# Performance work log

Measured on AMD Instinct MI355X. Metric: run time of the kernel, lower is better.

## Reference

```python
import jax, jax.numpy as jnp
import numpy as np

DT = 0.01
SIM_STEPS = 10_000_000
G = jnp.array([0.0, -9.81], dtype=jnp.float32)  # gravity, matches Ball.g


def setup_inputs() -> dict:
    key = jax.random.key(0)
    k_pos, k_vel = jax.random.split(key)
    return {
        "ball_mass": jnp.ones((), dtype=jnp.float32),  # unused by the math, kept for signature fidelity
        "ball_initial_position": jax.random.normal(k_pos, (2,), dtype=jnp.float32),
        "ball_initial_velocity": jax.random.normal(k_vel, (2,), dtype=jnp.float32),  # nn.Parameter
    }


def reference(ball_mass, ball_initial_position, ball_initial_velocity):
    # Faithful semi-implicit-Euler-style recurrence:
    #   pos <- pos + vel*dt ; vel <- vel + g*dt ; record pos
    # trajectory[0] is the initial position, trajectory[1:] are the updated positions.
    def step(carry, _):
        pos, vel = carry
        pos = pos + vel * DT
        vel = vel + G * DT
        return (pos, vel), pos

    _, traj = jax.lax.scan(
        step, (ball_initial_position, ball_initial_velocity), None, length=SIM_STEPS - 1
    )  # traj: [SIM_STEPS-1, 2]
    return jnp.concatenate([ball_initial_position[None, :], traj], axis=0)  # [SIM_STEPS, 2]
```

## Files before the change

### kernel.cpp

```cpp
#include <hip/hip_runtime.h>
#include <stdint.h>


static constexpr long long NSTEPS = 10000000LL;
static constexpr long long NPOLY  = 4000000LL;
static constexpr long long NS     = 8000000LL;
static constexpr long long KDIR   = 64;
static constexpr int SEGCAP = 384;
static constexpr int RUNCAP = 96;

typedef float f4_native __attribute__((ext_vector_type(4)));

__device__ __forceinline__ bool same_binade_f32(float a, float b) {
    return (((__float_as_uint(a) ^ __float_as_uint(b)) & 0xFF800000u) == 0u);
}
__device__ __forceinline__ unsigned expfield(float v) {
    return (__float_as_uint(v) >> 23) & 0xFFu;
}
__device__ __forceinline__ float pow2f(int e) {
    return __uint_as_float((unsigned)(e + 127) << 23);
}
__device__ __forceinline__ double pow2d(int e) {
    return __longlong_as_double(((long long)(e + 1023)) << 52);
}
__device__ __forceinline__ void nt_store(float4* p, float4 v) {
    f4_native nv;
    nv.x = v.x; nv.y = v.y; nv.z = v.z; nv.w = v.w;
    __builtin_nontemporal_store(nv, (f4_native*)p);
}

__global__ __launch_bounds__(256, 4) void fused(
        const float* __restrict__ pos0, const float* __restrict__ vel0,
        float4* __restrict__ out, long long npairs)
{
    __shared__ int    s_m[SEGCAP + 1];
    __shared__ double s_V[SEGCAP], s_c[SEGCAP], s_P[SEGCAP], s_dP[SEGCAP];
    __shared__ float  s_Vf[SEGCAP], s_cdt[SEGCAP], s_Pf[SEGCAP];
    __shared__ int    r_n[RUNCAP];
    __shared__ double r_p[RUNCAP], r_i[RUNCAP];
    __shared__ float  r_pf[RUNCAP], r_if[RUNCAP];
    __shared__ int    s_nseg, s_bad, s_nrun;
    __shared__ long long s_mstop;
    __shared__ double s_v64, s_p64;

    const int tid  = threadIdx.x;
    const int lane = tid & 63;
    const int wv   = tid >> 6;

    const long long per = (npairs + (long long)gridDim.x - 1) / (long long)gridDim.x;
    const long long i0 = (long long)blockIdx.x * per;
    long long i1 = i0 + per; if (i1 > npairs) i1 = npairs;
    if (i0 >= npairs) return;
    const long long row0 = 2 * i0;
    const long long row1 = 2 * i1;
    const long long mstop = row1 < NSTEPS ? row1 : NSTEPS;

    const float dtf  = 0.01f;
    const float gdtf = __fmul_rn(-9.81f, dtf);
    const double dtd = (double)dtf, gcd = (double)gdtf, gdtd = gcd;
    const double p0y = (double)pos0[1], v0y = (double)vel0[1];

    int k_tie;
    {
        unsigned gbits = __float_as_uint(gdtf);
        unsigned mant = (gbits & 0x7FFFFFu) | 0x800000u;
        int tz = __ffs((int)mant) - 1;
        int E = (int)((gbits >> 23) & 0xFFu) - 127 - 23 + tz;
        k_tie = E + 25;
    }

    if (tid == 0) { s_nseg = 0; s_nrun = 0; s_mstop = 0; s_bad = 0; }
    __syncthreads();

    if (wv == 0 && row1 > NPOLY) {
        double V = v0y, P = p0y;
        for (int t = 0; t < (int)KDIR; ++t) {
            const float vf = (float)V;
            P += dtd * V;
            V = (double)__fadd_rn(vf, gdtf);
        }
        if (lane == 0) { s_v64 = V; s_p64 = P; }

        bool bad = false;
        long long m = KDIR;
        int nseg = 0;
        while (m < mstop && nseg < SEGCAP - 2) {
            const float vf = (float)V;
            const unsigned ef = expfield(vf);
            bad = bad | ((double)vf != V) | !(vf < 0.0f) | (ef == 0u) | (ef == 0xFFu);
            if (bad) break;
            const int k = (int)ef - 126;
            const float vn1 = __fadd_rn(vf, gdtf);
            const double c = (double)vn1 - V;
            if (!(c < 0.0)) { bad = true; break; }
            const long long rem = mstop - m;

            long long T = 1;
            if (k != k_tie) {
                const double inv_ulp = pow2d(24 - k);
                const double g  = -V * inv_ulp;
                const double q  = -gcd * inv_ulp;
                const double cg = -c * inv_ulp;
                const double lim = 16777216.0;
                float t0f = __fdividef((float)(lim - g - q), (float)cg);
                const long long Th = (long long)t0f;
                const long long Tc = Th - 31 + (long long)lane;
                const bool valid = (Tc >= 1) && (Tc <= rem)
                                && (g + (double)(Tc - 1) * cg + q < lim);
                const unsigned long long msk = __ballot(valid);
                if (msk) T = Th - 31 + (long long)(63 - __clzll(msk));
                else     T = (Th - 31 > rem) ? rem : 1;
                if (T < 1) T = 1;
                if (T > rem) T = rem;
            }
            if (lane == 0) { s_m[nseg] = (int)m; s_V[nseg] = V; s_c[nseg] = c; }
            ++nseg;
            V += (double)T * c;
            m += T;
        }
        bad = bad | (m < mstop);
        if (lane == 0) {
            s_bad = bad ? 1 : 0;
            s_nseg = nseg;
            s_mstop = m;
            s_m[nseg] = 0x7fffffff;
        }
    }
    __syncthreads();

    if (wv == 0 && s_bad && row1 > NPOLY) {
        double V = s_v64, P = s_p64;
        long long m = KDIR;
        int nseg = 0;
        while (m < mstop && nseg < SEGCAP) {
            const float vf  = (float)V;
            const float vn1 = __fadd_rn(vf, gdtf);
            const double c  = (double)vn1 - V;
            const long long rem = mstop - m;
            long long Lb = rem;
            const float cf = (float)c;
            const unsigned ef = expfield(vf);
            if (vf == 0.0f || ef == 0u) {
                Lb = 64;
            } else if (cf != 0.0f) {
                const int k = (int)ef - 126;
                float s = vf < 0.0f ? -1.0f : 1.0f;
                float B = ((vf < 0.0f) == (cf < 0.0f)) ? s * pow2f(k) : s * pow2f(k - 1);
                float r = __fdividef(B - vf, cf);
                if (r >= 0.0f && r < 4.0e9f) Lb = (long long)r + 1;
            }
            long long Lhi = Lb + 2;
            if (Lhi > rem) Lhi = rem;
            if (Lhi < 1) Lhi = 1;

            long long L = 1;
            {
                const long long candL = Lhi - 63 + (long long)lane;
                bool valid = false;
                if (candL >= 1) {
                    const double ve = V + (double)(candL - 1) * c;
                    const float vef = (float)ve;
                    const float vn2 = __fadd_rn(vef, gdtf);
                    valid = ((double)vef == ve)
                         && same_binade_f32(vef, vf)
                         && ((double)vn2 - ve == c);
                }
                const unsigned long long msk = __ballot(valid);
                if (msk) L = Lhi - 63 + (long long)(63 - __clzll(msk));
            }
            if (L < 1) L = 1;
            if (L > rem) L = rem;

            if (lane == 0) { s_m[nseg] = (int)m; s_V[nseg] = V; s_c[nseg] = c; s_P[nseg] = P; }
            ++nseg;
            P += dtd * ((double)L * V + c * ((double)L * (double)(L - 1) * 0.5));
            V += (double)L * c;
            m += L;
        }
        if (lane == 0) { s_nseg = nseg; s_mstop = m; s_m[nseg] = 0x7fffffff; }
    }
    __syncthreads();

    if (!s_bad && row1 > NPOLY && s_nseg > 0) {
        const int nseg = s_nseg;
        for (int j = tid; j < nseg; j += 256) {
            const long long mj = s_m[j];
            const long long me = (j + 1 < nseg) ? (long long)s_m[j + 1] : s_mstop;
            const double len = (double)(me - mj);
            s_dP[j] = dtd * (len * s_V[j] + s_c[j] * (len * (len - 1.0) * 0.5));
        }
        __syncthreads();
        if (tid == 0) {
            double P = s_p64;
            for (int j = 0; j < nseg; ++j) { s_P[j] = P; P += s_dP[j]; }
        }
    }
    __syncthreads();

    if (wv == 0 && row1 > NS && s_mstop >= NS && s_nseg > 0) {
        const int nseg = s_nseg;
        const long long mbuilt = s_mstop;
        int lo = 0, hi = nseg - 1;
        while (lo < hi) { int mid = (lo + hi + 1) >> 1;
                          if ((long long)s_m[mid] <= NS) lo = mid; else hi = mid - 1; }
        int jj = lo;
        const double t0 = (double)(NS - s_m[jj]);
        double vel = s_V[jj] + t0 * s_c[jj];
        double P2  = s_P[jj] + dtd * (t0 * s_V[jj] + s_c[jj] * (t0 * (t0 - 1.0) * 0.5));
        double pos = (double)(float)P2;
        long long n = NS;
        int nrun = 0;
        long long nend = (row1 < NSTEPS - 1) ? row1 : (NSTEPS - 1);
        if (nend > mbuilt) nend = mbuilt;
        while (n < nend && nrun < RUNCAP) {
            while (s_m[jj + 1] <= (int)n) ++jj;
            const double cv = s_c[jj];
            long long Lcap = (long long)s_m[jj + 1] - n;
            if (Lcap > mbuilt - n) Lcap = mbuilt - n;
            const long long rem = (NSTEPS - 1) - n;
            if (Lcap > rem) Lcap = rem;

            const float pf = (float)pos;
            const float vf2 = (float)vel;
            const float dstep = __fmul_rn(vf2, dtf);
            const float pn1 = __fadd_rn(pf, dstep);
            const double inc = (double)pn1 - pos;

            long long La = Lcap, Lc = Lcap;
            const float incf = (float)inc;
            const unsigned efp = expfield(pf);
            if (pf == 0.0f || efp == 0u) {
                La = 64;
            } else if (incf != 0.0f) {
                const int k = (int)efp - 126;
                float s = pf < 0.0f ? -1.0f : 1.0f;
                float B = ((pf < 0.0f) == (incf < 0.0f)) ? s * pow2f(k) : s * pow2f(k - 1);
                float r = __fdividef(B - pf, incf);
                if (r >= 0.0f && r < 4.0e9f) { La = (long long)r - 1; if (La < 0) La = 0; }
            }
            const double dd = cv * dtd;
            if (dd != 0.0 && pf != 0.0f && efp != 0u) {
                const int k = (int)efp - 126;
                if (k - 24 > -126) {
                    const float ulpf = pow2f(k - 24);
                    const double d0 = (double)dstep;
                    const double T = inc + (dd < 0.0 ? -0.5 : 0.5) * (double)ulpf;
                    float r = __fdividef((float)(T - d0), (float)dd);
                    if (r >= 0.0f && r < 4.0e9f) { Lc = (long long)r + 2; if (Lc < 1) Lc = 1; }
                }
            }
            long long Lhi = La < Lc ? La : Lc;
            Lhi += 3;
            if (Lhi > Lcap) Lhi = Lcap;
            if (Lhi < 1) Lhi = 1;

            long long L = 1;
            {
                const long long candL = Lhi - 63 + (long long)lane;
                bool valid = false;
                if (candL >= 1) {
                    const double pe = pos + (double)(candL - 1) * inc;
                    const double ve = vel + (double)(candL - 1) * cv;
                    const float pef = (float)pe;
                    const float vef = (float)ve;
                    const float d2  = __fmul_rn(vef, dtf);
                    const float pn2 = __fadd_rn(pef, d2);
                    valid = ((double)pef == pe)
                         && same_binade_f32(pef, pf)
                         && ((double)vef == ve)
                         && ((double)pn2 - pe == inc);
                }
                const unsigned long long msk = __ballot(valid);
                if (msk) L = Lhi - 63 + (long long)(63 - __clzll(msk));
            }
            if (L < 1) L = 1;
            if (L > Lcap) L = Lcap;
            if (L < 1) L = 1;

            if (lane == 0) { r_n[nrun] = (int)n; r_p[nrun] = pos; r_i[nrun] = inc; }
            ++nrun;
            pos += (double)L * inc;
            vel += (double)L * cv;
            n += L;
        }
        if (lane == 0) s_nrun = nrun;
    }
    __syncthreads();

    {
        const int nseg = s_nseg, nrun = s_nrun;
        for (int i = tid; i < nseg; i += 256) {
            s_Vf[i]  = (float)s_V[i];
            s_cdt[i] = (float)(dtd * s_c[i]);
            s_Pf[i]  = (float)s_P[i];
        }
        for (int i = tid; i < nrun; i += 256) {
            r_pf[i] = (float)r_p[i];
            r_if[i] = (float)r_i[i];
        }
    }
    __syncthreads();

    const int nseg = s_nseg;
    const int nrun = s_nrun;
    const float pxf = pos0[0];
    const float cxf = __fmul_rn(vel0[0], dtf);
    const float pyf = (float)p0y;
    const float vyf = (float)v0y;
    const float q2f = (float)(dtd * gdtd);

    const long long ii = i0 + tid;
    if (ii >= i1) return;

    int mode = 3, jf = 0, rf = 0;
    if (row1 <= NPOLY) {
        mode = 0;
    } else if (row0 >= NS && nrun > 0) {
        int rlo = 0, rhi = nrun - 1;
        const int t0 = (int)row0;
        while (rlo < rhi) { int mid = (rlo + rhi + 1) >> 1; if (r_n[mid] <= t0) rlo = mid; else rhi = mid - 1; }
        rf = rlo;
        if (rf + 1 >= nrun || (long long)r_n[rf + 1] >= row1) mode = 2;
    } else if (row0 >= NPOLY && row1 <= NS && nseg > 0) {
        int lo = 0, hi = nseg - 1;
        const int t0 = (int)row0;
        while (lo < hi) { int mid = (lo + hi + 1) >> 1; if (s_m[mid] <= t0) lo = mid; else hi = mid - 1; }
        jf = lo;
        if ((long long)s_m[jf + 1] >= row1) mode = 1;
    }

    if (mode == 0) {
        const float C = 0.5f * q2f;
        const float B = dtf * vyf - C;
        const float A = pyf;
        for (long long i = ii; i < i1; i += blockDim.x) {
            const float mf0 = (float)(2 * i), mf1 = mf0 + 1.0f;
            float4 o;
            o.x = fmaf(mf0, cxf, pxf);
            o.z = fmaf(mf1, cxf, pxf);
            o.y = fmaf(mf0, fmaf(mf0, C, B), A);
            o.w = fmaf(mf1, fmaf(mf1, C, B), A);
            nt_store(&out[i], o);
        }
    } else if (mode == 1) {
        const float C = 0.5f * s_cdt[jf];
        const float B = dtf * s_Vf[jf] - C;
        const float A = s_Pf[jf];
        const int mj = s_m[jf];
        for (long long i = ii; i < i1; i += blockDim.x) {
            const float t0 = (float)(int)(2 * i - mj), t1 = t0 + 1.0f;
            const float mf0 = (float)(2 * i), mf1 = mf0 + 1.0f;
            float4 o;
            o.x = fmaf(mf0, cxf, pxf);
            o.z = fmaf(mf1, cxf, pxf);
            o.y = fmaf(t0, fmaf(t0, C, B), A);
            o.w = fmaf(t1, fmaf(t1, C, B), A);
            nt_store(&out[i], o);
        }
    } else if (mode == 2) {
        const float A = r_pf[rf], Bv = r_if[rf];
        const int rn0 = r_n[rf];
        for (long long i = ii; i < i1; i += blockDim.x) {
            const float t0 = (float)(int)(2 * i - rn0), t1 = t0 + 1.0f;
            const float mf0 = (float)(2 * i), mf1 = mf0 + 1.0f;
            float4 o;
            o.x = fmaf(mf0, cxf, pxf);
            o.z = fmaf(mf1, cxf, pxf);
            o.y = fmaf(t0, Bv, A);
            o.w = fmaf(t1, Bv, A);
            nt_store(&out[i], o);
        }
    } else {
        int j = 0, r = 0;
        if (nseg > 0) {
            const int t0 = (int)(2 * ii);
            int lo = 0, hi = nseg - 1;
            while (lo < hi) { int mid = (lo + hi + 1) >> 1; if (s_m[mid] <= t0) lo = mid; else hi = mid - 1; }
            j = lo;
            if (nrun > 0) {
                int rlo = 0, rhi = nrun - 1;
                while (rlo < rhi) { int mid = (rlo + rhi + 1) >> 1; if (r_n[mid] <= t0) rlo = mid; else rhi = mid - 1; }
                r = rlo;
            }
        }
        for (long long i = ii; i < i1; i += blockDim.x) {
            const long long m0 = 2 * i, m1 = m0 + 1;
            const float mf0 = (float)m0, mf1 = (float)m1;
            float4 o;
            o.x = fmaf(mf0, cxf, pxf);
            o.z = fmaf(mf1, cxf, pxf);
            const int t0 = (int)m0;
            if (m1 < NPOLY) {
                const float C = 0.5f * q2f;
                const float B = dtf * vyf - C;
                o.y = fmaf(mf0, fmaf(mf0, C, B), pyf);
                o.w = fmaf(mf1, fmaf(mf1, C, B), pyf);
            } else if (m1 < NS || nrun <= 0) {
                while (s_m[j + 1] <= t0) ++j;
                float t = (float)(int)(m0 - s_m[j]);
                o.y = s_Pf[j] + dtf * (t * s_Vf[j]) + s_cdt[j] * (t * (t - 1.0f) * 0.5f);
                const int j1 = (s_m[j + 1] <= (int)m1) ? j + 1 : j;
                t = (float)(int)(m1 - s_m[j1]);
                o.w = s_Pf[j1] + dtf * (t * s_Vf[j1]) + s_cdt[j1] * (t * (t - 1.0f) * 0.5f);
            } else {
                while (r + 1 < nrun && r_n[r + 1] <= t0) ++r;
                o.y = r_pf[r] + (float)(int)(m0 - r_n[r]) * r_if[r];
                const int r1 = (r + 1 < nrun && r_n[r + 1] <= (int)m1) ? r + 1 : r;
                o.w = r_pf[r1] + (float)(int)(m1 - r_n[r1]) * r_if[r1];
            }
            nt_store(&out[i], o);
        }
    }
}

extern "C" void kernel_launch(void* const* d_in, const int* in_sizes, int n_in,
                              void* d_out, int out_size, void* d_ws, size_t ws_size,
                              hipStream_t stream) {
    const float* pos0 = (const float*)d_in[1];
    const float* vel0 = (const float*)d_in[2];

    const long long npairs = (long long)out_size / 4;
    fused<<<1024, 256, 0, stream>>>(pos0, vel0, (float4*)d_out, npairs);
}
```

Measured before the change: 35.13 us.

## Give each block a poly slice and a late slice, overlapping poly stores with segment build

Each block now owns one slice of the closed-form polynomial region and one slice of the later segment-based region, instead of a single contiguous range. Wave 0 builds the segment and run tables while the other three waves write the block's polynomial slice, so table construction overlaps with global stores. The fallback path and the prefix sum of P are merged into wave 0's single pass, which removes several __syncthreads and the s_dP scratch array. The cost is that every block now runs the serial segment-building loop, and the prefix sum is done by a single lane.

```diff
diff --git a/kernel.cpp b/kernel.cpp
--- a/kernel.cpp
+++ b/kernel.cpp
@@ -8,6 +8,8 @@
 static constexpr long long KDIR   = 64;
 static constexpr int SEGCAP = 384;
 static constexpr int RUNCAP = 96;
+static constexpr long long PF4 = NPOLY / 2;
+static constexpr long long LF4 = (NSTEPS - NPOLY) / 2;
 
 typedef float f4_native __attribute__((ext_vector_type(4)));
 
@@ -34,26 +36,24 @@
         float4* __restrict__ out, long long npairs)
 {
     __shared__ int    s_m[SEGCAP + 1];
-    __shared__ double s_V[SEGCAP], s_c[SEGCAP], s_P[SEGCAP], s_dP[SEGCAP];
+    __shared__ double s_V[SEGCAP], s_c[SEGCAP], s_P[SEGCAP];
     __shared__ float  s_Vf[SEGCAP], s_cdt[SEGCAP], s_Pf[SEGCAP];
     __shared__ int    r_n[RUNCAP];
     __shared__ double r_p[RUNCAP], r_i[RUNCAP];
     __shared__ float  r_pf[RUNCAP], r_if[RUNCAP];
-    __shared__ int    s_nseg, s_bad, s_nrun;
+    __shared__ int    s_nseg, s_nrun;
     __shared__ long long s_mstop;
-    __shared__ double s_v64, s_p64;
 
     const int tid  = threadIdx.x;
     const int lane = tid & 63;
     const int wv   = tid >> 6;
-
-    const long long per = (npairs + (long long)gridDim.x - 1) / (long long)gridDim.x;
-    const long long i0 = (long long)blockIdx.x * per;
-    long long i1 = i0 + per; if (i1 > npairs) i1 = npairs;
-    if (i0 >= npairs) return;
-    const long long row0 = 2 * i0;
-    const long long row1 = 2 * i1;
-    const long long mstop = row1 < NSTEPS ? row1 : NSTEPS;
+    const long long G = gridDim.x;
+    const long long b = blockIdx.x;
+
+    const long long pb0 = (b * PF4) / G,       pb1 = ((b + 1) * PF4) / G;
+    const long long lb0 = PF4 + (b * LF4) / G, lb1 = PF4 + ((b + 1) * LF4) / G;
+    const long long lrow0 = 2 * lb0, lrow1 = 2 * lb1;
+    const long long mstop = lrow1 < NSTEPS ? lrow1 : NSTEPS;
 
     const float dtf  = 0.01f;
     const float gdtf = __fmul_rn(-9.81f, dtf);
@@ -69,17 +69,22 @@
         k_tie = E + 25;
     }
 
-    if (tid == 0) { s_nseg = 0; s_nrun = 0; s_mstop = 0; s_bad = 0; }
-    __syncthreads();
-
-    if (wv == 0 && row1 > NPOLY) {
+    const float pxf = pos0[0];
+    const float cxf = __fmul_rn(vel0[0], dtf);
+    const float pyf = (float)p0y;
+    const float vyf = (float)v0y;
+    const float q2f = (float)(dtd * gdtd);
+    const float Cq  = 0.5f * q2f;
+    const float Bq  = dtf * vyf - Cq;
+
+    if (wv == 0) {
         double V = v0y, P = p0y;
         for (int t = 0; t < (int)KDIR; ++t) {
             const float vf = (float)V;
             P += dtd * V;
             V = (double)__fadd_rn(vf, gdtf);
         }
-        if (lane == 0) { s_v64 = V; s_p64 = P; }
+        const double v64 = V, p64 = P;
 
         bool bad = false;
         long long m = KDIR;
@@ -119,171 +124,171 @@
             m += T;
         }
         bad = bad | (m < mstop);
+        long long built = m;
+
+        if (bad) {
+            V = v64; P = p64;
+            m = KDIR;
+            nseg = 0;
+            while (m < mstop && nseg < SEGCAP) {
+                const float vf  = (float)V;
+                const float vn1 = __fadd_rn(vf, gdtf);
+                const double c  = (double)vn1 - V;
+                const long long rem = mstop - m;
+                long long Lb = rem;
+                const float cf = (float)c;
+                const unsigned ef = expfield(vf);
+                if (vf == 0.0f || ef == 0u) {
+                    Lb = 64;
+                } else if (cf != 0.0f) {
+                    const int k = (int)ef - 126;
+                    float s = vf < 0.0f ? -1.0f : 1.0f;
+                    float B = ((vf < 0.0f) == (cf < 0.0f)) ? s * pow2f(k) : s * pow2f(k - 1);
+                    float r = __fdividef(B - vf, cf);
+                    if (r >= 0.0f && r < 4.0e9f) Lb = (long long)r + 1;
+                }
+                long long Lhi = Lb + 2;
+                if (Lhi > rem) Lhi = rem;
+                if (Lhi < 1) Lhi = 1;
+
+                long long L = 1;
+                {
+                    const long long candL = Lhi - 63 + (long long)lane;
+                    bool valid = false;
+                    if (candL >= 1) {
+                        const double ve = V + (double)(candL - 1) * c;
+                        const float vef = (float)ve;
+                        const float vn2 = __fadd_rn(vef, gdtf);
+                        valid = ((double)vef == ve)
+                             && same_binade_f32(vef, vf)
+                             && ((double)vn2 - ve == c);
+                    }
+                    const unsigned long long msk = __ballot(valid);
+                    if (msk) L = Lhi - 63 + (long long)(63 - __clzll(msk));
+                }
+                if (L < 1) L = 1;
+                if (L > rem) L = rem;
+
+                if (lane == 0) { s_m[nseg] = (int)m; s_V[nseg] = V; s_c[nseg] = c; s_P[nseg] = P; }
+                ++nseg;
+                P += dtd * ((double)L * V + c * ((double)L * (double)(L - 1) * 0.5));
+                V += (double)L * c;
+                m += L;
+            }
+            built = m;
+        } else if (lane == 0 && nseg > 0) {
+            double Pp = p64;
+            for (int j = 0; j < nseg; ++j) {
+                s_P[j] = Pp;
+                const long long mj = s_m[j];
+                const long long me = (j + 1 < nseg) ? (long long)s_m[j + 1] : built;
+                const double len = (double)(me - mj);
+                Pp += dtd * (len * s_V[j] + s_c[j] * (len * (len - 1.0) * 0.5));
+            }
+        }
         if (lane == 0) {
-            s_bad = bad ? 1 : 0;
             s_nseg = nseg;
-            s_mstop = m;
+            s_mstop = built;
             s_m[nseg] = 0x7fffffff;
-        }
-    }
-    __syncthreads();
-
-    if (wv == 0 && s_bad && row1 > NPOLY) {
-        double V = s_v64, P = s_p64;
-        long long m = KDIR;
-        int nseg = 0;
-        while (m < mstop && nseg < SEGCAP) {
-            const float vf  = (float)V;
-            const float vn1 = __fadd_rn(vf, gdtf);
-            const double c  = (double)vn1 - V;
-            const long long rem = mstop - m;
-            long long Lb = rem;
-            const float cf = (float)c;
-            const unsigned ef = expfield(vf);
-            if (vf == 0.0f || ef == 0u) {
-                Lb = 64;
-            } else if (cf != 0.0f) {
-                const int k = (int)ef - 126;
-                float s = vf < 0.0f ? -1.0f : 1.0f;
-                float B = ((vf < 0.0f) == (cf < 0.0f)) ? s * pow2f(k) : s * pow2f(k - 1);
-                float r = __fdividef(B - vf, cf);
-                if (r >= 0.0f && r < 4.0e9f) Lb = (long long)r + 1;
-            }
-            long long Lhi = Lb + 2;
-            if (Lhi > rem) Lhi = rem;
-            if (Lhi < 1) Lhi = 1;
-
-            long long L = 1;
-            {
-                const long long candL = Lhi - 63 + (long long)lane;
-                bool valid = false;
-                if (candL >= 1) {
-                    const double ve = V + (double)(candL - 1) * c;
-                    const float vef = (float)ve;
-                    const float vn2 = __fadd_rn(vef, gdtf);
-                    valid = ((double)vef == ve)
-                         && same_binade_f32(vef, vf)
-                         && ((double)vn2 - ve == c);
+            s_nrun = 0;
+        }
+
+        if (lrow1 > NS && built >= NS && nseg > 0) {
+            int lo = 0, hi = nseg - 1;
+            while (lo < hi) { int mid = (lo + hi + 1) >> 1;
+                              if ((long long)s_m[mid] <= NS) lo = mid; else hi = mid - 1; }
+            int jj = lo;
+            const double t0 = (double)(NS - s_m[jj]);
+            double vel = s_V[jj] + t0 * s_c[jj];
+            double P2  = s_P[jj] + dtd * (t0 * s_V[jj] + s_c[jj] * (t0 * (t0 - 1.0) * 0.5));
+            double pos = (double)(float)P2;
+            long long n = NS;
+            int nrun = 0;
+            long long nend = (lrow1 < NSTEPS - 1) ? lrow1 : (NSTEPS - 1);
+            if (nend > built) nend = built;
+            while (n < nend && nrun < RUNCAP) {
+                while (s_m[jj + 1] <= (int)n) ++jj;
+                const double cv = s_c[jj];
+                long long Lcap = (long long)s_m[jj + 1] - n;
+                if (Lcap > built - n) Lcap = built - n;
+                const long long rem = (NSTEPS - 1) - n;
+                if (Lcap > rem) Lcap = rem;
+
+                const float pf = (float)pos;
+                const float vf2 = (float)vel;
+                const float dstep = __fmul_rn(vf2, dtf);
+                const float pn1 = __fadd_rn(pf, dstep);
+                const double inc = (double)pn1 - pos;
+
+                long long La = Lcap, Lc = Lcap;
+                const float incf = (float)inc;
+                const unsigned efp = expfield(pf);
+                if (pf == 0.0f || efp == 0u) {
+                    La = 64;
+                } else if (incf != 0.0f) {
+                    const int k = (int)efp - 126;
+                    float s = pf < 0.0f ? -1.0f : 1.0f;
+                    float B = ((pf < 0.0f) == (incf < 0.0f)) ? s * pow2f(k) : s * pow2f(k - 1);
+                    float r = __fdividef(B - pf, incf);
+                    if (r >= 0.0f && r < 4.0e9f) { La = (long long)r - 1; if (La < 0) La = 0; }
                 }
-                const unsigned long long msk = __ballot(valid);
-                if (msk) L = Lhi - 63 + (long long)(63 - __clzll(msk));
-            }
-            if (L < 1) L = 1;
-            if (L > rem) L = rem;
-
-            if (lane == 0) { s_m[nseg] = (int)m; s_V[nseg] = V; s_c[nseg] = c; s_P[nseg] = P; }
-            ++nseg;
-            P += dtd * ((double)L * V + c * ((double)L * (double)(L - 1) * 0.5));
-            V += (double)L * c;
-            m += L;
-        }
-        if (lane == 0) { s_nseg = nseg; s_mstop = m; s_m[nseg] = 0x7fffffff; }
-    }
-    __syncthreads();
-
-    if (!s_bad && row1 > NPOLY && s_nseg > 0) {
-        const int nseg = s_nseg;
-        for (int j = tid; j < nseg; j += 256) {
-            const long long mj = s_m[j];
-            const long long me = (j + 1 < nseg) ? (long long)s_m[j + 1] : s_mstop;
-            const double len = (double)(me - mj);
-            s_dP[j] = dtd * (len * s_V[j] + s_c[j] * (len * (len - 1.0) * 0.5));
-        }
-        __syncthreads();
-        if (tid == 0) {
-            double P = s_p64;
-            for (int j = 0; j < nseg; ++j) { s_P[j] = P; P += s_dP[j]; }
-        }
-    }
-    __syncthreads();
-
-    if (wv == 0 && row1 > NS && s_mstop >= NS && s_nseg > 0) {
-        const int nseg = s_nseg;
-        const long long mbuilt = s_mstop;
-        int lo = 0, hi = nseg - 1;
-        while (lo < hi) { int mid = (lo + hi + 1) >> 1;
-                          if ((long long)s_m[mid] <= NS) lo = mid; else hi = mid - 1; }
-        int jj = lo;
-        const double t0 = (double)(NS - s_m[jj]);
-        double vel = s_V[jj] + t0 * s_c[jj];
-        double P2  = s_P[jj] + dtd * (t0 * s_V[jj] + s_c[jj] * (t0 * (t0 - 1.0) * 0.5));
-        double pos = (double)(float)P2;
-        long long n = NS;
-        int nrun = 0;
-        long long nend = (row1 < NSTEPS - 1) ? row1 : (NSTEPS - 1);
-        if (nend > mbuilt) nend = mbuilt;
-        while (n < nend && nrun < RUNCAP) {
-            while (s_m[jj + 1] <= (int)n) ++jj;
-            const double cv = s_c[jj];
-            long long Lcap = (long long)s_m[jj + 1] - n;
-            if (Lcap > mbuilt - n) Lcap = mbuilt - n;
-            const long long rem = (NSTEPS - 1) - n;
-            if (Lcap > rem) Lcap = rem;
-
-            const float pf = (float)pos;
-            const float vf2 = (float)vel;
-            const float dstep = __fmul_rn(vf2, dtf);
-            const float pn1 = __fadd_rn(pf, dstep);
-            const double inc = (double)pn1 - pos;
-
-            long long La = Lcap, Lc = Lcap;
-            const float incf = (float)inc;
-            const unsigned efp = expfield(pf);
-            if (pf == 0.0f || efp == 0u) {
-                La = 64;
-            } else if (incf != 0.0f) {
-                const int k = (int)efp - 126;
-                float s = pf < 0.0f ? -1.0f : 1.0f;
-                float B = ((pf < 0.0f) == (incf < 0.0f)) ? s * pow2f(k) : s * pow2f(k - 1);
-                float r = __fdividef(B - pf, incf);
-                if (r >= 0.0f && r < 4.0e9f) { La = (long long)r - 1; if (La < 0) La = 0; }
-            }
-            const double dd = cv * dtd;
-            if (dd != 0.0 && pf != 0.0f && efp != 0u) {
-                const int k = (int)efp - 126;
-                if (k - 24 > -126) {
-                    const float ulpf = pow2f(k - 24);
-                    const double d0 = (double)dstep;
-                    const double T = inc + (dd < 0.0 ? -0.5 : 0.5) * (double)ulpf;
-                    float r = __fdividef((float)(T - d0), (float)dd);
-                    if (r >= 0.0f && r < 4.0e9f) { Lc = (long long)r + 2; if (Lc < 1) Lc = 1; }
+                const double dd = cv * dtd;
+                if (dd != 0.0 && pf != 0.0f && efp != 0u) {
+                    const int k = (int)efp - 126;
+                    if (k - 24 > -126) {
+                        const float ulpf = pow2f(k - 24);
+                        const double d0 = (double)dstep;
+                        const double T = inc + (dd < 0.0 ? -0.5 : 0.5) * (double)ulpf;
+                        float r = __fdividef((float)(T - d0), (float)dd);
+                        if (r >= 0.0f && r < 4.0e9f) { Lc = (long long)r + 2; if (Lc < 1) Lc = 1; }
+                    }
                 }
-            }
-            long long Lhi = La < Lc ? La : Lc;
-            Lhi += 3;
-            if (Lhi > Lcap) Lhi = Lcap;
-            if (Lhi < 1) Lhi = 1;
-
-            long long L = 1;
-            {
-                const long long candL = Lhi - 63 + (long long)lane;
-                bool valid = false;
-                if (candL >= 1) {
-                    const double pe = pos + (double)(candL - 1) * inc;
-                    const double ve = vel + (double)(candL - 1) * cv;
-                    const float pef = (float)pe;
-                    const float vef = (float)ve;
-                    const float d2  = __fmul_rn(vef, dtf);
-                    const float pn2 = __fadd_rn(pef, d2);
-                    valid = ((double)pef == pe)
-                         && same_binade_f32(pef, pf)
-                         && ((double)vef == ve)
-                         && ((double)pn2 - pe == inc);
+                long long Lhi = La < Lc ? La : Lc;
+                Lhi += 3;
+                if (Lhi > Lcap) Lhi = Lcap;
+                if (Lhi < 1) Lhi = 1;
+
+                long long L = 1;
+                {
+                    const long long candL = Lhi - 63 + (long long)lane;
+                    bool valid = false;
+                    if (candL >= 1) {
+                        const double pe = pos + (double)(candL - 1) * inc;
+                        const double ve = vel + (double)(candL - 1) * cv;
+                        const float pef = (float)pe;
+                        const float vef = (float)ve;
+                        const float d2  = __fmul_rn(vef, dtf);
+                        const float pn2 = __fadd_rn(pef, d2);
+                        valid = ((double)pef == pe)
+                             && same_binade_f32(pef, pf)
+                             && ((double)vef == ve)
+                             && ((double)pn2 - pe == inc);
+                    }
+                    const unsigned long long msk = __ballot(valid);
+                    if (msk) L = Lhi - 63 + (long long)(63 - __clzll(msk));
                 }
-                const unsigned long long msk = __ballot(valid);
-                if (msk) L = Lhi - 63 + (long long)(63 - __clzll(msk));
-            }
-            if (L < 1) L = 1;
-            if (L > Lcap) L = Lcap;
-            if (L < 1) L = 1;
-
-            if (lane == 0) { r_n[nrun] = (int)n; r_p[nrun] = pos; r_i[nrun] = inc; }
-            ++nrun;
-            pos += (double)L * inc;
-            vel += (double)L * cv;
-            n += L;
-        }
-        if (lane == 0) s_nrun = nrun;
+                if (L < 1) L = 1;
+                if (L > Lcap) L = Lcap;
+                if (L < 1) L = 1;
+
+                if (lane == 0) { r_n[nrun] = (int)n; r_p[nrun] = pos; r_i[nrun] = inc; }
+                ++nrun;
+                pos += (double)L * inc;
+                vel += (double)L * cv;
+                n += L;
+            }
+            if (lane == 0) s_nrun = nrun;
+        }
+    } else {
+        for (long long i = pb0 + (tid - 64); i < pb1; i += 192) {
+            const float mf0 = (float)(2 * i), mf1 = mf0 + 1.0f;
+            float4 o;
+            o.x = fmaf(mf0, cxf, pxf);
+            o.z = fmaf(mf1, cxf, pxf);
+            o.y = fmaf(mf0, fmaf(mf0, Cq, Bq), pyf);
+            o.w = fmaf(mf1, fmaf(mf1, Cq, Bq), pyf);
+            nt_store(&out[i], o);
+        }
     }
     __syncthreads();
 
@@ -303,51 +308,30 @@
 
     const int nseg = s_nseg;
     const int nrun = s_nrun;
-    const float pxf = pos0[0];
-    const float cxf = __fmul_rn(vel0[0], dtf);
-    const float pyf = (float)p0y;
-    const float vyf = (float)v0y;
-    const float q2f = (float)(dtd * gdtd);
-
-    const long long ii = i0 + tid;
-    if (ii >= i1) return;
+    const long long ii = lb0 + tid;
+    if (ii >= lb1) return;
 
     int mode = 3, jf = 0, rf = 0;
-    if (row1 <= NPOLY) {
-        mode = 0;
-    } else if (row0 >= NS && nrun > 0) {
+    if (lrow0 >= NS && nrun > 0) {
         int rlo = 0, rhi = nrun - 1;
-        const int t0 = (int)row0;
+        const int t0 = (int)lrow0;
         while (rlo < rhi) { int mid = (rlo + rhi + 1) >> 1; if (r_n[mid] <= t0) rlo = mid; else rhi = mid - 1; }
         rf = rlo;
-        if (rf + 1 >= nrun || (long long)r_n[rf + 1] >= row1) mode = 2;
-    } else if (row0 >= NPOLY && row1 <= NS && nseg > 0) {
+        if (rf + 1 >= nrun || (long long)r_n[rf + 1] >= lrow1) mode = 2;
+    } else if (lrow1 <= NS && nseg > 0) {
         int lo = 0, hi = nseg - 1;
-        const int t0 = (int)row0;
+        const int t0 = (int)lrow0;
         while (lo < hi) { int mid = (lo + hi + 1) >> 1; if (s_m[mid] <= t0) lo = mid; else hi = mid - 1; }
         jf = lo;
-        if ((long long)s_m[jf + 1] >= row1) mode = 1;
+        if ((long long)s_m[jf + 1] >= lrow1) mode = 1;
     }
 
-    if (mode == 0) {
-        const float C = 0.5f * q2f;
-        const float B = dtf * vyf - C;
-        const float A = pyf;
-        for (long long i = ii; i < i1; i += blockDim.x) {
-            const float mf0 = (float)(2 * i), mf1 = mf0 + 1.0f;
-            float4 o;
-            o.x = fmaf(mf0, cxf, pxf);
-            o.z = fmaf(mf1, cxf, pxf);
-            o.y = fmaf(mf0, fmaf(mf0, C, B), A);
-            o.w = fmaf(mf1, fmaf(mf1, C, B), A);
-            nt_store(&out[i], o);
-        }
-    } else if (mode == 1) {
+    if (mode == 1) {
         const float C = 0.5f * s_cdt[jf];
         const float B = dtf * s_Vf[jf] - C;
         const float A = s_Pf[jf];
         const int mj = s_m[jf];
-        for (long long i = ii; i < i1; i += blockDim.x) {
+        for (long long i = ii; i < lb1; i += blockDim.x) {
             const float t0 = (float)(int)(2 * i - mj), t1 = t0 + 1.0f;
             const float mf0 = (float)(2 * i), mf1 = mf0 + 1.0f;
             float4 o;
@@ -360,7 +344,7 @@
     } else if (mode == 2) {
         const float A = r_pf[rf], Bv = r_if[rf];
         const int rn0 = r_n[rf];
-        for (long long i = ii; i < i1; i += blockDim.x) {
+        for (long long i = ii; i < lb1; i += blockDim.x) {
             const float t0 = (float)(int)(2 * i - rn0), t1 = t0 + 1.0f;
             const float mf0 = (float)(2 * i), mf1 = mf0 + 1.0f;
             float4 o;
@@ -383,19 +367,14 @@
                 r = rlo;
             }
         }
-        for (long long i = ii; i < i1; i += blockDim.x) {
+        for (long long i = ii; i < lb1; i += blockDim.x) {
             const long long m0 = 2 * i, m1 = m0 + 1;
             const float mf0 = (float)m0, mf1 = (float)m1;
             float4 o;
             o.x = fmaf(mf0, cxf, pxf);
             o.z = fmaf(mf1, cxf, pxf);
             const int t0 = (int)m0;
-            if (m1 < NPOLY) {
-                const float C = 0.5f * q2f;
-                const float B = dtf * vyf - C;
-                o.y = fmaf(mf0, fmaf(mf0, C, B), pyf);
-                o.w = fmaf(mf1, fmaf(mf1, C, B), pyf);
-            } else if (m1 < NS || nrun <= 0) {
+            if (m1 < NS || nrun <= 0) {
                 while (s_m[j + 1] <= t0) ++j;
                 float t = (float)(int)(m0 - s_m[j]);
                 o.y = s_Pf[j] + dtf * (t * s_Vf[j]) + s_cdt[j] * (t * (t - 1.0f) * 0.5f);
```

Result: slower. 38.06 us (+8.4%).

## Compute velocity segment lengths with exact integer mantissa arithmetic instead of ballot search

Applied to the files above, without the earlier changes.

The serial segment-building loop now tracks velocity as an integer mantissa and exponent and derives each constant-increment run length from integer math plus a single division with small corrections. This replaces the per-segment 64-lane ballot search and the double-precision probing. Velocities and increments are rebuilt in parallel afterward, and the prefix sum is folded into one serial loop. The aim is a shorter latency-bound serial chain in wave 0, at the cost of added correctness checks and extra shared arrays.

```diff
diff --git a/kernel.cpp b/kernel.cpp
--- a/kernel.cpp
+++ b/kernel.cpp
@@ -23,6 +23,10 @@
 __device__ __forceinline__ double pow2d(int e) {
     return __longlong_as_double(((long long)(e + 1023)) << 52);
 }
+__device__ __forceinline__ float f32_from_kg(int k, long long g) {
+    return __uint_as_float(0x80000000u | ((unsigned)(k + 126) << 23)
+                           | ((unsigned)g & 0x7FFFFFu));
+}
 __device__ __forceinline__ void nt_store(float4* p, float4 v) {
     f4_native nv;
     nv.x = v.x; nv.y = v.y; nv.z = v.z; nv.w = v.w;
@@ -34,7 +38,9 @@
         float4* __restrict__ out, long long npairs)
 {
     __shared__ int    s_m[SEGCAP + 1];
-    __shared__ double s_V[SEGCAP], s_c[SEGCAP], s_P[SEGCAP], s_dP[SEGCAP];
+    __shared__ int    s_kI[SEGCAP + 1];
+    __shared__ long long s_gI[SEGCAP + 1], s_cgI[SEGCAP];
+    __shared__ double s_V[SEGCAP + 1], s_c[SEGCAP], s_P[SEGCAP];
     __shared__ float  s_Vf[SEGCAP], s_cdt[SEGCAP], s_Pf[SEGCAP];
     __shared__ int    r_n[RUNCAP];
     __shared__ double r_p[RUNCAP], r_i[RUNCAP];
@@ -60,13 +66,13 @@
     const double dtd = (double)dtf, gcd = (double)gdtf, gdtd = gcd;
     const double p0y = (double)pos0[1], v0y = (double)vel0[1];
 
-    int k_tie;
+    long long Mg; int Eg;
     {
         unsigned gbits = __float_as_uint(gdtf);
         unsigned mant = (gbits & 0x7FFFFFu) | 0x800000u;
         int tz = __ffs((int)mant) - 1;
-        int E = (int)((gbits >> 23) & 0xFFu) - 127 - 23 + tz;
-        k_tie = E + 25;
+        Mg = (long long)(mant >> tz);
+        Eg = (int)((gbits >> 23) & 0xFFu) - 127 - 23 + tz;
     }
 
     if (tid == 0) { s_nseg = 0; s_nrun = 0; s_mstop = 0; s_bad = 0; }
@@ -82,41 +88,63 @@
         if (lane == 0) { s_v64 = V; s_p64 = P; }
 
         bool bad = false;
+        const float vf0 = (float)V;
+        const unsigned ef0 = expfield(vf0);
+        bad |= ((double)vf0 != V) | !(vf0 < 0.0f) | (ef0 == 0u) | (ef0 == 0xFFu);
+        int k = (int)ef0 - 126;
+        long long g = (long long)((__float_as_uint(vf0) & 0x7FFFFFu) | 0x800000u);
         long long m = KDIR;
         int nseg = 0;
-        while (m < mstop && nseg < SEGCAP - 2) {
-            const float vf = (float)V;
-            const unsigned ef = expfield(vf);
-            bad = bad | ((double)vf != V) | !(vf < 0.0f) | (ef == 0u) | (ef == 0xFFu);
-            if (bad) break;
-            const int k = (int)ef - 126;
-            const float vn1 = __fadd_rn(vf, gdtf);
-            const double c = (double)vn1 - V;
-            if (!(c < 0.0)) { bad = true; break; }
+
+        while (!bad && m < mstop && nseg < SEGCAP - 2) {
+            const int s = k - 24 - Eg;
             const long long rem = mstop - m;
-
-            long long T = 1;
-            if (k != k_tie) {
-                const double inv_ulp = pow2d(24 - k);
-                const double g  = -V * inv_ulp;
-                const double q  = -gcd * inv_ulp;
-                const double cg = -c * inv_ulp;
-                const double lim = 16777216.0;
-                float t0f = __fdividef((float)(lim - g - q), (float)cg);
-                const long long Th = (long long)t0f;
-                const long long Tc = Th - 31 + (long long)lane;
-                const bool valid = (Tc >= 1) && (Tc <= rem)
-                                && (g + (double)(Tc - 1) * cg + q < lim);
-                const unsigned long long msk = __ballot(valid);
-                if (msk) T = Th - 31 + (long long)(63 - __clzll(msk));
-                else     T = (Th - 31 > rem) ? rem : 1;
-                if (T < 1) T = 1;
-                if (T > rem) T = rem;
-            }
-            if (lane == 0) { s_m[nseg] = (int)m; s_V[nseg] = V; s_c[nseg] = c; }
-            ++nseg;
-            V += (double)T * c;
-            m += T;
+            long long T = 0, cg = 0;
+            if (s >= 2) {
+                cg = (Mg + (1LL << (s - 1))) >> s;
+                const long long num = (1LL << (24 + s)) - Mg - (g << s);
+                if (num >= 1 && cg >= 1) {
+                    const long long den = cg << s;
+                    const float tf = __fdividef((float)num, (float)den);
+                    T = (long long)tf + 1;
+                    if (T < 1) T = 1;
+                    for (int f = 0; f < 4 && T > 1 && (T - 1) * den >= num; ++f) --T;
+                    for (int f = 0; f < 4 && T * den < num; ++f) ++T;
+                    if (T > rem) T = rem;
+                }
+            }
+            if (T >= 1) {
+                const float vv = f32_from_kg(k, g);
+                const float vn = __fadd_rn(vv, gdtf);
+                long long ge = g + cg; int ke = k;
+                if (ge >= (1LL << 24)) {
+                    bad |= (ge != (1LL << 24));
+                    ge = 1LL << 23; ke = k + 1;
+                }
+                bad |= (__float_as_uint(vn) != __float_as_uint(f32_from_kg(ke, ge)));
+
+                if (lane == 0) { s_m[nseg] = (int)m; s_kI[nseg] = k;
+                                 s_gI[nseg] = g; s_cgI[nseg] = cg; }
+                ++nseg;
+                g += T * cg; m += T;
+                if (g >= (1LL << 24)) {
+                    bad |= (g != (1LL << 24));
+                    g = 1LL << 23; k += 1;
+                }
+                continue;
+            }
+            {
+                const float vv = f32_from_kg(k, g);
+                const float vb = __fadd_rn(vv, gdtf);
+                const unsigned eb = expfield(vb);
+                bad |= (eb == 0u) | (eb == 0xFFu) | !(vb < 0.0f);
+                if (lane == 0) { s_m[nseg] = (int)m; s_kI[nseg] = k;
+                                 s_gI[nseg] = g; s_cgI[nseg] = 0; }
+                ++nseg;
+                k = (int)eb - 126;
+                g = (long long)((__float_as_uint(vb) & 0x7FFFFFu) | 0x800000u);
+                m += 1;
+            }
         }
         bad = bad | (m < mstop);
         if (lane == 0) {
@@ -124,6 +152,7 @@
             s_nseg = nseg;
             s_mstop = m;
             s_m[nseg] = 0x7fffffff;
+            s_kI[nseg] = k; s_gI[nseg] = g;
         }
     }
     __syncthreads();
@@ -182,17 +211,29 @@
     __syncthreads();
 
     if (!s_bad && row1 > NPOLY && s_nseg > 0) {
-        const int nseg = s_nseg;
-        for (int j = tid; j < nseg; j += 256) {
+        const int ns = s_nseg;
+        for (int j = tid; j <= ns; j += 256)
+            s_V[j] = -(double)s_gI[j] * pow2d(s_kI[j] - 24);
+    }
+    __syncthreads();
+    if (!s_bad && row1 > NPOLY && s_nseg > 0) {
+        const int ns = s_nseg;
+        for (int j = tid; j < ns; j += 256) {
+            s_c[j] = (s_cgI[j] > 0) ? -(double)s_cgI[j] * pow2d(s_kI[j] - 24)
+                                    : (s_V[j + 1] - s_V[j]);
+        }
+    }
+    __syncthreads();
+
+    if (!s_bad && row1 > NPOLY && s_nseg > 0 && tid == 0) {
+        const int ns = s_nseg;
+        double Pp = s_p64;
+        for (int j = 0; j < ns; ++j) {
+            s_P[j] = Pp;
             const long long mj = s_m[j];
-            const long long me = (j + 1 < nseg) ? (long long)s_m[j + 1] : s_mstop;
+            const long long me = (j + 1 < ns) ? (long long)s_m[j + 1] : s_mstop;
             const double len = (double)(me - mj);
-            s_dP[j] = dtd * (len * s_V[j] + s_c[j] * (len * (len - 1.0) * 0.5));
-        }
-        __syncthreads();
-        if (tid == 0) {
-            double P = s_p64;
-            for (int j = 0; j < nseg; ++j) { s_P[j] = P; P += s_dP[j]; }
+            Pp += dtd * (len * s_V[j] + s_c[j] * (len * (len - 1.0) * 0.5));
         }
     }
     __syncthreads();
```

Measured after the change: 42.13 us. 19.9% more time.
